# Performance work log

Hardware: AMD Instinct MI355X
Metric: run time of the kernel (lower is better)

## Reference

```python
import jax, jax.numpy as jnp
import numpy as np

EPS = 1e-06
SIGMA_C = 2.0


def setup_inputs() -> dict:
    key = jax.random.key(0)
    k1, k2 = jax.random.split(key)
    B, L, D, T = 16, 512, 256, 2048
    text = jax.random.normal(k1, (B, L, D), dtype=jnp.float32)
    durs = jax.random.randint(k2, (B, L), 0, 8, dtype=jnp.int64)
    return {"text": text, "durs": durs, "total_time": T}


def reference(text, durs, total_time):
    # text: [B, L, D], durs: [B, L] int, total_time: static python int T
    d = durs.astype(jnp.float32)
    # NOTE: faithful to original: mean = durs/2 + cumsum(durs) (cumsum includes current dur)
    mean = d / 2.0 + jnp.cumsum(d, axis=-1)            # [B, L]
    sigma = d / SIGMA_C + EPS                          # [B, L]
    t = jnp.arange(total_time, dtype=jnp.float32) + 0.5  # [T]
    # Normal pdf evaluated at t: exp(log_prob) = exp(-0.5 z^2) / (sigma * sqrt(2 pi))
    z = (t[None, :, None] - mean[:, None, :]) / sigma[:, None, :]  # [B, T, L]
    inv_norm = 1.0 / (sigma[:, None, :] * jnp.sqrt(2.0 * jnp.pi))
    probs = jnp.exp(-0.5 * z * z) * inv_norm           # [B, T, L]
    probs = probs / (probs.sum(-1, keepdims=True) + EPS)
    return jnp.einsum("btl,bld->btd", probs, text)     # [B, T, D]
```

## Files before the change

kernel.cpp:

```cpp
#include <hip/hip_runtime.h>
#include <math.h>

#define L 512
#define TILE_T 16
#define NTHREADS 256
#define NACT_MAX 160
#define ZWIN 14.5f

static constexpr float EPS = 1e-6f;
static constexpr float INV_SQRT_2PI = 0.39894228040143267794f;

__global__ __launch_bounds__(NTHREADS, 8) void ge_kernel(
    const float* __restrict__ text,
    const int*   __restrict__ durs,
    float*       __restrict__ out,
    int B, int D, int T, int tilesPerB)
{
    __shared__ float s_lmean[NACT_MAX];
    __shared__ float s_lisig[NACT_MAX];
    __shared__ int   s_lrow[NACT_MAX];
    __shared__ float s_probs[NACT_MAX][TILE_T];
    __shared__ float s_wtot[4];
    __shared__ int   s_wcnt[4];
    __shared__ float s_wsum[4][TILE_T];
    __shared__ float s_norm[TILE_T];

    const int tid  = threadIdx.x;
    const int lane = tid & 63;
    const int wid  = tid >> 6;
    const int blk  = blockIdx.x;
    const int b    = blk / tilesPerB;
    const int t0   = (blk % tilesPerB) * TILE_T;

    const int l0 = 2 * tid;
    const float d0 = (float)durs[b * L + l0];
    const float d1 = (float)durs[b * L + l0 + 1];
    const float pairsum = d0 + d1;

    float v = pairsum;
    #pragma unroll
    for (int off = 1; off < 64; off <<= 1) {
        float n = __shfl_up(v, off, 64);
        if (lane >= off) v += n;
    }
    if (lane == 63) s_wtot[wid] = v;
    __syncthreads();
    float wpre = 0.f;
    for (int w = 0; w < wid; ++w) wpre += s_wtot[w];
    const float excl = wpre + v - pairsum;

    const float cum0  = excl + d0;
    const float cum1  = cum0 + d1;
    const float mean0 = cum0 + 0.5f * d0;
    const float mean1 = cum1 + 0.5f * d1;
    const float sig0  = 0.5f * d0 + EPS;
    const float sig1  = 0.5f * d1 + EPS;
    const float isig0 = 1.0f / sig0;
    const float isig1 = 1.0f / sig1;

    const float tlo = (float)t0 + 0.5f;
    const float thi = (float)t0 + (float)TILE_T - 0.5f;
    const float r0 = ZWIN * sig0;
    const float r1 = ZWIN * sig1;
    const bool act0 = (d0 >= 1.f) && (mean0 + r0 >= tlo) && (mean0 - r0 <= thi);
    const bool act1 = (d1 >= 1.f) && (mean1 + r1 >= tlo) && (mean1 - r1 <= thi);

    const unsigned long long m0 = __ballot(act0);
    const unsigned long long m1 = __ballot(act1);
    const unsigned long long lt = (lane == 0) ? 0ull : ((~0ull) >> (64 - lane));
    const int off_in_wave = __popcll(m0 & lt) + __popcll(m1 & lt);
    const int cnt_wave = __popcll(m0) + __popcll(m1);
    if (lane == 0) s_wcnt[wid] = cnt_wave;
    __syncthreads();
    int base_w = 0;
    for (int w = 0; w < wid; ++w) base_w += s_wcnt[w];
    const int nact = s_wcnt[0] + s_wcnt[1] + s_wcnt[2] + s_wcnt[3];

    if (act0) {
        const int i = base_w + off_in_wave;
        s_lrow[i] = l0; s_lmean[i] = mean0; s_lisig[i] = isig0;
    }
    if (act1) {
        const int i = base_w + off_in_wave + (act0 ? 1 : 0);
        s_lrow[i] = l0 + 1; s_lmean[i] = mean1; s_lisig[i] = isig1;
    }
    __syncthreads();

    float psum = 0.f;
    const int   mytt = tid & 15;
    const float myt  = (float)(t0 + mytt) + 0.5f;
    const int total = nact * TILE_T;
    for (int idx = tid; idx < total; idx += NTHREADS) {
        const int i = idx >> 4;
        const float z = (myt - s_lmean[i]) * s_lisig[i];
        const float p = __expf(-0.5f * z * z) * s_lisig[i] * INV_SQRT_2PI;
        s_probs[i][mytt] = p;
        psum += p;
    }
    psum += __shfl_xor(psum, 16, 64);
    psum += __shfl_xor(psum, 32, 64);
    if (lane < 16) s_wsum[wid][lane] = psum;
    __syncthreads();
    if (tid < TILE_T) {
        const float s = s_wsum[0][tid] + s_wsum[1][tid] + s_wsum[2][tid] + s_wsum[3][tid];
        s_norm[tid] = 1.0f / (s + EPS);
    }
    __syncthreads();

    float4 a0 = {0,0,0,0}, a1 = {0,0,0,0}, a2 = {0,0,0,0}, a3 = {0,0,0,0};
    const float* tbase = text + (size_t)b * L * D + (lane << 2);
    #pragma unroll 2
    for (int i = 0; i < nact; ++i) {
        const int l = s_lrow[i];
        const float4 val = *(const float4*)(tbase + (size_t)l * D);
        const float4 p   = *(const float4*)&s_probs[i][wid << 2];
        a0.x += p.x * val.x; a0.y += p.x * val.y; a0.z += p.x * val.z; a0.w += p.x * val.w;
        a1.x += p.y * val.x; a1.y += p.y * val.y; a1.z += p.y * val.z; a1.w += p.y * val.w;
        a2.x += p.z * val.x; a2.y += p.z * val.y; a2.z += p.z * val.z; a2.w += p.z * val.w;
        a3.x += p.w * val.x; a3.y += p.w * val.y; a3.z += p.w * val.z; a3.w += p.w * val.w;
    }

    const float4 nrm = *(const float4*)&s_norm[wid << 2];
    const int tt0 = t0 + (wid << 2);
    float* obase = out + ((size_t)b * T + tt0) * D + (lane << 2);
    if (tt0 + 0 < T) { float4 o = {a0.x*nrm.x, a0.y*nrm.x, a0.z*nrm.x, a0.w*nrm.x}; *(float4*)(obase + 0*(size_t)D) = o; }
    if (tt0 + 1 < T) { float4 o = {a1.x*nrm.y, a1.y*nrm.y, a1.z*nrm.y, a1.w*nrm.y}; *(float4*)(obase + 1*(size_t)D) = o; }
    if (tt0 + 2 < T) { float4 o = {a2.x*nrm.z, a2.y*nrm.z, a2.z*nrm.z, a2.w*nrm.z}; *(float4*)(obase + 2*(size_t)D) = o; }
    if (tt0 + 3 < T) { float4 o = {a3.x*nrm.w, a3.y*nrm.w, a3.z*nrm.w, a3.w*nrm.w}; *(float4*)(obase + 3*(size_t)D) = o; }
}

extern "C" void kernel_launch(void* const* d_in, const int* in_sizes, int n_in,
                              void* d_out, int out_size, void* d_ws, size_t ws_size,
                              hipStream_t stream) {
    const float* text = (const float*)d_in[0];
    const int*   durs = (const int*)d_in[1];
    float*       out  = (float*)d_out;

    const int BL = in_sizes[1];
    const int D  = in_sizes[0] / BL;
    const int B  = BL / L;
    const int T  = out_size / (B * D);
    const int tilesPerB = (T + TILE_T - 1) / TILE_T;

    ge_kernel<<<dim3(B * tilesPerB), dim3(NTHREADS), 0, stream>>>(
        text, durs, out, B, D, T, tilesPerB);
}
```

Before: 18.16 us.

## Double time tile to 32 rows per block and prefetch text rows in accumulation loop

Raises the time tile from 16 to 32 steps so each wave accumulates 8 output rows instead of 4. Every text row fetched from global memory is therefore reused across twice as many time steps, and the grid shrinks by half. It also adds a software prefetch of the next active text row and lowers the occupancy hint to 6 blocks per CU. The costs are more accumulator registers and lower occupancy. The larger window may also hold more active rows, while NACT_MAX was cut to 136, which risks overflow on long-duration inputs.

```diff
diff --git a/kernel.cpp b/kernel.cpp
--- a/kernel.cpp
+++ b/kernel.cpp
@@ -2,15 +2,15 @@
 #include <math.h>
 
 #define L 512
-#define TILE_T 16
+#define TILE_T 32
 #define NTHREADS 256
-#define NACT_MAX 160
+#define NACT_MAX 136
 #define ZWIN 14.5f
 
 static constexpr float EPS = 1e-6f;
 static constexpr float INV_SQRT_2PI = 0.39894228040143267794f;
 
-__global__ __launch_bounds__(NTHREADS, 8) void ge_kernel(
+__global__ __launch_bounds__(NTHREADS, 6) void ge_kernel(
     const float* __restrict__ text,
     const int*   __restrict__ durs,
     float*       __restrict__ out,
@@ -87,19 +87,19 @@
     __syncthreads();
 
     float psum = 0.f;
-    const int   mytt = tid & 15;
+    const int   mytt = tid & 31;
     const float myt  = (float)(t0 + mytt) + 0.5f;
     const int total = nact * TILE_T;
     for (int idx = tid; idx < total; idx += NTHREADS) {
-        const int i = idx >> 4;
-        const float z = (myt - s_lmean[i]) * s_lisig[i];
-        const float p = __expf(-0.5f * z * z) * s_lisig[i] * INV_SQRT_2PI;
+        const int i = idx >> 5;
+        const float isg = s_lisig[i];
+        const float z = (myt - s_lmean[i]) * isg;
+        const float p = __expf(-0.5f * z * z) * isg * INV_SQRT_2PI;
         s_probs[i][mytt] = p;
         psum += p;
     }
-    psum += __shfl_xor(psum, 16, 64);
     psum += __shfl_xor(psum, 32, 64);
-    if (lane < 16) s_wsum[wid][lane] = psum;
+    if (lane < 32) s_wsum[wid][lane] = psum;
     __syncthreads();
     if (tid < TILE_T) {
         const float s = s_wsum[0][tid] + s_wsum[1][tid] + s_wsum[2][tid] + s_wsum[3][tid];
@@ -107,26 +107,41 @@
     }
     __syncthreads();
 
-    float4 a0 = {0,0,0,0}, a1 = {0,0,0,0}, a2 = {0,0,0,0}, a3 = {0,0,0,0};
+    float4 a[8];
+    #pragma unroll
+    for (int k = 0; k < 8; ++k) a[k] = make_float4(0.f, 0.f, 0.f, 0.f);
+
     const float* tbase = text + (size_t)b * L * D + (lane << 2);
-    #pragma unroll 2
-    for (int i = 0; i < nact; ++i) {
-        const int l = s_lrow[i];
-        const float4 val = *(const float4*)(tbase + (size_t)l * D);
-        const float4 p   = *(const float4*)&s_probs[i][wid << 2];
-        a0.x += p.x * val.x; a0.y += p.x * val.y; a0.z += p.x * val.z; a0.w += p.x * val.w;
-        a1.x += p.y * val.x; a1.y += p.y * val.y; a1.z += p.y * val.z; a1.w += p.y * val.w;
-        a2.x += p.z * val.x; a2.y += p.z * val.y; a2.z += p.z * val.z; a2.w += p.z * val.w;
-        a3.x += p.w * val.x; a3.y += p.w * val.y; a3.z += p.w * val.z; a3.w += p.w * val.w;
+    const float* sprow = &s_probs[0][wid << 3];
+    if (nact > 0) {
+        float4 vnext = *(const float4*)(tbase + (size_t)s_lrow[0] * D);
+        for (int i = 0; i < nact; ++i) {
+            const float4 val = vnext;
+            if (i + 1 < nact)
+                vnext = *(const float4*)(tbase + (size_t)s_lrow[i + 1] * D);
+            const float4 p0 = *(const float4*)(sprow + i * TILE_T + 0);
+            const float4 p1 = *(const float4*)(sprow + i * TILE_T + 4);
+            const float pw[8] = {p0.x, p0.y, p0.z, p0.w, p1.x, p1.y, p1.z, p1.w};
+            #pragma unroll
+            for (int k = 0; k < 8; ++k) {
+                a[k].x += pw[k] * val.x;
+                a[k].y += pw[k] * val.y;
+                a[k].z += pw[k] * val.z;
+                a[k].w += pw[k] * val.w;
+            }
+        }
     }
 
-    const float4 nrm = *(const float4*)&s_norm[wid << 2];
-    const int tt0 = t0 + (wid << 2);
+    const int tt0 = t0 + (wid << 3);
     float* obase = out + ((size_t)b * T + tt0) * D + (lane << 2);
-    if (tt0 + 0 < T) { float4 o = {a0.x*nrm.x, a0.y*nrm.x, a0.z*nrm.x, a0.w*nrm.x}; *(float4*)(obase + 0*(size_t)D) = o; }
-    if (tt0 + 1 < T) { float4 o = {a1.x*nrm.y, a1.y*nrm.y, a1.z*nrm.y, a1.w*nrm.y}; *(float4*)(obase + 1*(size_t)D) = o; }
-    if (tt0 + 2 < T) { float4 o = {a2.x*nrm.z, a2.y*nrm.z, a2.z*nrm.z, a2.w*nrm.z}; *(float4*)(obase + 2*(size_t)D) = o; }
-    if (tt0 + 3 < T) { float4 o = {a3.x*nrm.w, a3.y*nrm.w, a3.z*nrm.w, a3.w*nrm.w}; *(float4*)(obase + 3*(size_t)D) = o; }
+    #pragma unroll
+    for (int j = 0; j < 8; ++j) {
+        if (tt0 + j < T) {
+            const float n = s_norm[(wid << 3) + j];
+            const float4 o = make_float4(a[j].x * n, a[j].y * n, a[j].z * n, a[j].w * n);
+            *(float4*)(obase + (size_t)j * D) = o;
+        }
+    }
 }
 
 extern "C" void kernel_launch(void* const* d_in, const int* in_sizes, int n_in,
```

Measured after the change: 20.79 us. +14.5%, slower.

## Remap workgroups across XCDs and software-prefetch text rows in accumulation loop

Applied to the files above, without the earlier changes.

Remaps block indices so that consecutive time tiles of the same batch land on the same XCD, sharing that XCD's L2 for the text rows and durations. Replaces the unrolled accumulation loop with an explicit one-ahead prefetch of the next text row. Also removes the T bounds checks on the output stores and hoists a shared-memory load. The remap assumes the workgroup count divides by 8 and that T is a multiple of the tile size; otherwise tiles are skipped or stores go out of bounds.

```diff
diff --git a/kernel.cpp b/kernel.cpp
--- a/kernel.cpp
+++ b/kernel.cpp
@@ -6,6 +6,7 @@
 #define NTHREADS 256
 #define NACT_MAX 160
 #define ZWIN 14.5f
+#define NXCD 8
 
 static constexpr float EPS = 1e-6f;
 static constexpr float INV_SQRT_2PI = 0.39894228040143267794f;
@@ -14,7 +15,7 @@
     const float* __restrict__ text,
     const int*   __restrict__ durs,
     float*       __restrict__ out,
-    int B, int D, int T, int tilesPerB)
+    int B, int D, int T, int tilesPerB, int nwg)
 {
     __shared__ float s_lmean[NACT_MAX];
     __shared__ float s_lisig[NACT_MAX];
@@ -28,9 +29,11 @@
     const int tid  = threadIdx.x;
     const int lane = tid & 63;
     const int wid  = tid >> 6;
-    const int blk  = blockIdx.x;
-    const int b    = blk / tilesPerB;
-    const int t0   = (blk % tilesPerB) * TILE_T;
+
+    const int orig = blockIdx.x;
+    const int wg   = (orig & (NXCD - 1)) * (nwg / NXCD) + (orig >> 3);
+    const int b    = wg / tilesPerB;
+    const int t0   = (wg % tilesPerB) * TILE_T;
 
     const int l0 = 2 * tid;
     const float d0 = (float)durs[b * L + l0];
@@ -92,8 +95,9 @@
     const int total = nact * TILE_T;
     for (int idx = tid; idx < total; idx += NTHREADS) {
         const int i = idx >> 4;
-        const float z = (myt - s_lmean[i]) * s_lisig[i];
-        const float p = __expf(-0.5f * z * z) * s_lisig[i] * INV_SQRT_2PI;
+        const float isg = s_lisig[i];
+        const float z = (myt - s_lmean[i]) * isg;
+        const float p = __expf(-0.5f * z * z) * isg * INV_SQRT_2PI;
         s_probs[i][mytt] = p;
         psum += p;
     }
@@ -109,24 +113,27 @@
 
     float4 a0 = {0,0,0,0}, a1 = {0,0,0,0}, a2 = {0,0,0,0}, a3 = {0,0,0,0};
     const float* tbase = text + (size_t)b * L * D + (lane << 2);
-    #pragma unroll 2
-    for (int i = 0; i < nact; ++i) {
-        const int l = s_lrow[i];
-        const float4 val = *(const float4*)(tbase + (size_t)l * D);
-        const float4 p   = *(const float4*)&s_probs[i][wid << 2];
-        a0.x += p.x * val.x; a0.y += p.x * val.y; a0.z += p.x * val.z; a0.w += p.x * val.w;
-        a1.x += p.y * val.x; a1.y += p.y * val.y; a1.z += p.y * val.z; a1.w += p.y * val.w;
-        a2.x += p.z * val.x; a2.y += p.z * val.y; a2.z += p.z * val.z; a2.w += p.z * val.w;
-        a3.x += p.w * val.x; a3.y += p.w * val.y; a3.z += p.w * val.z; a3.w += p.w * val.w;
+    if (nact > 0) {
+        float4 vnext = *(const float4*)(tbase + (size_t)s_lrow[0] * D);
+        for (int i = 0; i < nact; ++i) {
+            const float4 val = vnext;
+            if (i + 1 < nact)
+                vnext = *(const float4*)(tbase + (size_t)s_lrow[i + 1] * D);
+            const float4 p = *(const float4*)&s_probs[i][wid << 2];
+            a0.x += p.x * val.x; a0.y += p.x * val.y; a0.z += p.x * val.z; a0.w += p.x * val.w;
+            a1.x += p.y * val.x; a1.y += p.y * val.y; a1.z += p.y * val.z; a1.w += p.y * val.w;
+            a2.x += p.z * val.x; a2.y += p.z * val.y; a2.z += p.z * val.z; a2.w += p.z * val.w;
+            a3.x += p.w * val.x; a3.y += p.w * val.y; a3.z += p.w * val.z; a3.w += p.w * val.w;
+        }
     }
 
     const float4 nrm = *(const float4*)&s_norm[wid << 2];
     const int tt0 = t0 + (wid << 2);
     float* obase = out + ((size_t)b * T + tt0) * D + (lane << 2);
-    if (tt0 + 0 < T) { float4 o = {a0.x*nrm.x, a0.y*nrm.x, a0.z*nrm.x, a0.w*nrm.x}; *(float4*)(obase + 0*(size_t)D) = o; }
-    if (tt0 + 1 < T) { float4 o = {a1.x*nrm.y, a1.y*nrm.y, a1.z*nrm.y, a1.w*nrm.y}; *(float4*)(obase + 1*(size_t)D) = o; }
-    if (tt0 + 2 < T) { float4 o = {a2.x*nrm.z, a2.y*nrm.z, a2.z*nrm.z, a2.w*nrm.z}; *(float4*)(obase + 2*(size_t)D) = o; }
-    if (tt0 + 3 < T) { float4 o = {a3.x*nrm.w, a3.y*nrm.w, a3.z*nrm.w, a3.w*nrm.w}; *(float4*)(obase + 3*(size_t)D) = o; }
+    { float4 o = {a0.x*nrm.x, a0.y*nrm.x, a0.z*nrm.x, a0.w*nrm.x}; *(float4*)(obase + 0*(size_t)D) = o; }
+    { float4 o = {a1.x*nrm.y, a1.y*nrm.y, a1.z*nrm.y, a1.w*nrm.y}; *(float4*)(obase + 1*(size_t)D) = o; }
+    { float4 o = {a2.x*nrm.z, a2.y*nrm.z, a2.z*nrm.z, a2.w*nrm.z}; *(float4*)(obase + 2*(size_t)D) = o; }
+    { float4 o = {a3.x*nrm.w, a3.y*nrm.w, a3.z*nrm.w, a3.w*nrm.w}; *(float4*)(obase + 3*(size_t)D) = o; }
 }
 
 extern "C" void kernel_launch(void* const* d_in, const int* in_sizes, int n_in,
@@ -141,7 +148,8 @@
     const int B  = BL / L;
     const int T  = out_size / (B * D);
     const int tilesPerB = (T + TILE_T - 1) / TILE_T;
+    const int nwg = B * tilesPerB;
 
-    ge_kernel<<<dim3(B * tilesPerB), dim3(NTHREADS), 0, stream>>>(
-        text, durs, out, B, D, T, tilesPerB);
+    ge_kernel<<<dim3(nwg), dim3(NTHREADS), 0, stream>>>(
+        text, durs, out, B, D, T, tilesPerB, nwg);
 }
```

Result: no change. 18.09 us (-0.4%).
